# Kernel optimization log

Measured on AMD Instinct MI355X. Metric: run time of the kernel, lower is better.

The kernel has to match this reference:

```python
import jax, jax.numpy as jnp
import numpy as np

NVAR, B, C, H, W = 3, 4, 256, 64, 64
C1 = C // 2          # dat channels (nc)
C2 = C - C1
HEADS = 4
HC = C1 // HEADS     # head channels
STRIDE = 4
KS = 4
HK, WK = H // STRIDE, W // STRIDE
NS = HK * WK         # n_sample
RPE_H, RPE_W = 2 * H - 1, 2 * W - 1
NPAIR = 3


def _grid_sample(img, grid):
    # img [B,C,Hi,Wi]; grid [B,Hg,Wg,2] = (x,y) in [-1,1]; bilinear, align_corners=True, zero-pad
    Bn, Cn, Hi, Wi = img.shape
    x = (grid[..., 0] + 1.0) * 0.5 * (Wi - 1)
    y = (grid[..., 1] + 1.0) * 0.5 * (Hi - 1)
    x0 = jnp.floor(x)
    y0 = jnp.floor(y)
    wx = x - x0
    wy = y - y0
    x0i = x0.astype(jnp.int32)
    y0i = y0.astype(jnp.int32)
    imt = img.transpose(0, 2, 3, 1)  # [B,Hi,Wi,C]
    bidx = jnp.arange(Bn)[:, None, None]

    def corner(yi, xi, wgt):
        ok = ((xi >= 0) & (xi < Wi) & (yi >= 0) & (yi < Hi)).astype(img.dtype)
        val = imt[bidx, jnp.clip(yi, 0, Hi - 1), jnp.clip(xi, 0, Wi - 1)]  # [B,Hg,Wg,C]
        return val * (wgt * ok)[..., None]

    out = (corner(y0i, x0i, (1 - wx) * (1 - wy))
           + corner(y0i, x0i + 1, wx * (1 - wy))
           + corner(y0i + 1, x0i, (1 - wx) * wy)
           + corner(y0i + 1, x0i + 1, wx * wy))
    return out.transpose(0, 3, 1, 2)  # [B,C,Hg,Wg]


def _ref_points(hk, wk):
    # normalized sampling-grid reference points, (y,x) order
    ry = (jnp.linspace(0.5, hk - 0.5, hk) / (hk - 1.0)) * 2.0 - 1.0
    rx = (jnp.linspace(0.5, wk - 0.5, wk) / (wk - 1.0)) * 2.0 - 1.0
    return jnp.stack(jnp.meshgrid(ry, rx, indexing='ij'), axis=-1)  # [hk,wk,2]


def _q_grid(h, w):
    gy = (jnp.arange(h, dtype=jnp.float32) / (h - 1.0)) * 2.0 - 1.0
    gx = (jnp.arange(w, dtype=jnp.float32) / (w - 1.0)) * 2.0 - 1.0
    return jnp.stack(jnp.meshgrid(gy, gx, indexing='ij'), axis=-1).reshape(h * w, 2)


def _conv1x1(x, w, b=None):
    y = jnp.einsum('oc,bchw->bohw', w, x)
    return y if b is None else y + b[None, :, None, None]


def _dat_block(q_in, kv_in, pWq, pbq, pWk, pbk, pWv, pbv, pWo, pbo,
               pdw_w, pdw_b, pln_g, pln_b, ppw_w, prpe):
    Bn = q_in.shape[0]
    q = _conv1x1(q_in, pWq, pbq)  # [B,C1,H,W]
    # offset net: depthwise 4x4 stride-4 conv -> channel LN -> GELU -> 1x1 conv to 2
    off = jax.lax.conv_general_dilated(
        q, pdw_w, (STRIDE, STRIDE), 'VALID',
        dimension_numbers=('NCHW', 'OIHW', 'NCHW'),
        feature_group_count=C1) + pdw_b[None, :, None, None]  # [B,C1,HK,WK]
    mu = off.mean(axis=1, keepdims=True)
    var = ((off - mu) ** 2).mean(axis=1, keepdims=True)
    off = (off - mu) * jax.lax.rsqrt(var + 1e-5) * pln_g[None, :, None, None] + pln_b[None, :, None, None]
    off = jax.nn.gelu(off, approximate=False)
    offset = _conv1x1(off, ppw_w).transpose(0, 2, 3, 1)  # [B,HK,WK,2] (dy,dx)
    # offset_range_factor = -1 -> no tanh scaling, clamp pos into [-1,1]
    pos = jnp.clip(offset + _ref_points(HK, WK)[None], -1.0, 1.0)  # [B,HK,WK,2]
    xs = _grid_sample(kv_in, pos[..., ::-1])  # sample kv at deformed points -> [B,C1,HK,WK]
    k = _conv1x1(xs, pWk, pbk).reshape(Bn, HEADS, HC, NS)
    v = _conv1x1(xs, pWv, pbv).reshape(Bn, HEADS, HC, NS)
    qh = q.reshape(Bn, HEADS, HC, H * W)
    attn = jnp.einsum('bhcm,bhcn->bhmn', qh, k) * (HC ** -0.5)  # [B,h,HW,NS]
    # relative position bias sampled from rpe table
    disp = (_q_grid(H, W)[None, :, None, :] - pos.reshape(Bn, 1, NS, 2)) * 0.5  # [B,HW,NS,2]
    rpe_b = jnp.broadcast_to(prpe[None], (Bn, HEADS, RPE_H, RPE_W))
    bias = _grid_sample(rpe_b, disp[..., ::-1])  # [B,h,HW,NS]
    attn = jax.nn.softmax(attn + bias, axis=-1)
    out = jnp.einsum('bhmn,bhcn->bhcm', attn, v).reshape(Bn, C1, H, W)
    return _conv1x1(out, pWo, pbo)


def _forward(xs, params):
    results = []
    num = 0
    for i in range(NVAR):
        res = xs[i]
        for j in range(i):
            attn_out = _dat_block(xs[i][:, :C1], xs[j][:, :C1],
                                  *(p[num] for p in params))
            # torch: res -= -cat(zeros[:,:C2], attn)  => add attn on channels C2:
            res = res.at[:, C2:].add(attn_out)
            num += 1
        results.append(res)
    return jnp.stack(results)  # [NVAR,B,C,H,W]


def setup_inputs() -> dict:
    key = jax.random.key(0)
    ks = jax.random.split(key, 4)
    d = {}
    for n, k in zip(['x0', 'x1', 'x2'], jax.random.split(ks[0], 3)):
        d[n] = jax.random.normal(k, (B, C, H, W), jnp.float32)

    def w(k, shape, s=0.02):
        return jax.random.normal(k, shape, jnp.float32) * s

    kk = jax.random.split(ks[1], 8)
    d['Wq'] = w(kk[0], (NPAIR, C1, C1))
    d['bq'] = jnp.zeros((NPAIR, C1), jnp.float32)
    d['Wk'] = w(kk[1], (NPAIR, C1, C1))
    d['bk'] = jnp.zeros((NPAIR, C1), jnp.float32)
    d['Wv'] = w(kk[2], (NPAIR, C1, C1))
    d['bv'] = jnp.zeros((NPAIR, C1), jnp.float32)
    d['Wo'] = w(kk[3], (NPAIR, C1, C1))
    d['bo'] = jnp.zeros((NPAIR, C1), jnp.float32)
    d['dw_w'] = w(kk[4], (NPAIR, C1, 1, KS, KS), 0.1)
    d['dw_b'] = jnp.zeros((NPAIR, C1), jnp.float32)
    d['ln_g'] = jnp.ones((NPAIR, C1), jnp.float32)
    d['ln_b'] = jnp.zeros((NPAIR, C1), jnp.float32)
    d['pw_w'] = w(kk[5], (NPAIR, 2, C1), 0.1)
    d['rpe'] = w(kk[6], (NPAIR, HEADS, RPE_H, RPE_W), 0.01)
    return d


def reference(x0, x1, x2, Wq, bq, Wk, bk, Wv, bv, Wo, bo,
              dw_w, dw_b, ln_g, ln_b, pw_w, rpe):
    params = (Wq, bq, Wk, bk, Wv, bv, Wo, bo, dw_w, dw_b, ln_g, ln_b, pw_w, rpe)
    out = _forward([x0, x1, x2], params)
    flow = jnp.zeros((NVAR, x0.shape[0]), out.dtype)
    return out, flow
```

## Files before the change

### kernel.cpp

```cpp
#include <hip/hip_runtime.h>
#include <math.h>

#define NVAR 3
#define BB 4
#define CC 256
#define C1 128
#define HEADS 4
#define HH 64
#define WW 64
#define HW 4096
#define RPE_W 127
#define NP 3
#define SCALE 0.17677669529663687f

typedef short bf16x8 __attribute__((ext_vector_type(8)));
typedef float f32x4 __attribute__((ext_vector_type(4)));
typedef __bf16 bf16x2 __attribute__((ext_vector_type(2)));

__device__ __forceinline__ unsigned short f2bf(float f) {
    unsigned int u = __float_as_uint(f);
    u += 0x7fffu + ((u >> 16) & 1u);
    return (unsigned short)(u >> 16);
}
__device__ __forceinline__ float bflo(unsigned u) { return __uint_as_float(u << 16); }
__device__ __forceinline__ float bfhi(unsigned u) { return __uint_as_float(u & 0xffff0000u); }

__device__ __forceinline__ float dot2bf(unsigned a, unsigned b, float c) {
#if __has_builtin(__builtin_amdgcn_fdot2_f32_bf16)
    return __builtin_amdgcn_fdot2_f32_bf16(__builtin_bit_cast(bf16x2, a),
                                           __builtin_bit_cast(bf16x2, b), c, false);
#else
    return c + bflo(a) * bflo(b) + bfhi(a) * bfhi(b);
#endif
}

__global__ __launch_bounds__(256) void prep_copy(const float* __restrict__ rpe,
                                                 const float* __restrict__ Wq,
                                                 const float* __restrict__ Wo,
                                                 const float* __restrict__ Wk,
                                                 const float* __restrict__ Wv,
                                                 const float* __restrict__ x0,
                                                 unsigned short* __restrict__ tabbf,
                                                 unsigned short* __restrict__ wqh,
                                                 unsigned short* __restrict__ wql,
                                                 unsigned short* __restrict__ woh,
                                                 unsigned short* __restrict__ wkh,
                                                 unsigned short* __restrict__ wvh,
                                                 float* __restrict__ out) {
    int blk = blockIdx.x;
    if (blk >= 24) {
        const long long n4 = (long long)BB * CC * HW / 4;
        long long i = (long long)(blk - 24) * 256 + threadIdx.x;
        const long long stride = 1024LL * 256;
        for (; i < n4 + 12; i += stride) {
            if (i < n4) ((float4*)out)[i] = ((const float4*)x0)[i];
            else out[3LL * BB * CC * HW + (i - n4)] = 0.f;
        }
        return;
    }
    if (blk < 12) {
        const float* src = rpe + (long long)blk * RPE_W * RPE_W;
        unsigned short* dst = tabbf + (long long)blk * 16384;
        for (int idx = threadIdx.x; idx < 16384; idx += 256) {
            int y = idx >> 7, x = idx & 127;
            float v = (y < RPE_W && x < RPE_W) ? src[y * RPE_W + x] : 0.f;
            dst[idx] = f2bf(v);
        }
    } else if (blk < 15) {
        int p = blk - 12;
        for (int i = threadIdx.x; i < 16384; i += 256) {
            float w = Wq[p * 16384 + i];
            unsigned short h = f2bf(w);
            wqh[p * 16384 + i] = h;
            wql[p * 16384 + i] = f2bf(w - bflo((unsigned)h));
        }
    } else if (blk < 18) {
        int p = blk - 15;
        for (int i = threadIdx.x; i < 16384; i += 256)
            woh[p * 16384 + i] = f2bf(Wo[p * 16384 + i]);
    } else if (blk < 21) {
        int p = blk - 18;
        for (int i = threadIdx.x; i < 16384; i += 256)
            wkh[p * 16384 + i] = f2bf(Wk[p * 16384 + i]);
    } else {
        int p = blk - 21;
        for (int i = threadIdx.x; i < 16384; i += 256)
            wvh[p * 16384 + i] = f2bf(Wv[p * 16384 + i]);
    }
}

__global__ __launch_bounds__(256) void conv_q(const float* __restrict__ x1,
                                              const float* __restrict__ x2,
                                              const unsigned short* __restrict__ wqh,
                                              const unsigned short* __restrict__ wql,
                                              const float* __restrict__ bq,
                                              float* __restrict__ qbuf,
                                              unsigned short* __restrict__ qbf,
                                              float* __restrict__ out) {
    __shared__ unsigned short qlds[4][16][136];
    int wid = threadIdx.x >> 6, lane = threadIdx.x & 63;
    int g = lane >> 4, lm = lane & 15;
    int gw = blockIdx.x * 4 + wid;
    int mt = gw & 255;
    int pb = gw >> 8;
    int p = pb >> 2, b = pb & 3;
    const float* X = ((p == 0) ? x1 : x2) + (long long)b * CC * HW;
    int m = mt * 16 + lm;
    float* outc = (p < 2)
        ? out + (((long long)((p + 1) * 4 + b)) * CC) * HW + m
        : nullptr;

    bf16x8 bhi[4], blo[4];
#pragma unroll
    for (int ksl = 0; ksl < 4; ksl++) {
        float v[8];
#pragma unroll
        for (int j = 0; j < 8; j++) {
            int k = ksl * 32 + 8 * g + j;
            v[j] = X[(long long)k * HW + m];
            if (outc) outc[(long long)k * HW] = v[j];
        }
        union { unsigned u[4]; bf16x8 v; } H, L;
#pragma unroll
        for (int t = 0; t < 4; t++) {
            unsigned short h0 = f2bf(v[2 * t]), h1 = f2bf(v[2 * t + 1]);
            unsigned short l0 = f2bf(v[2 * t] - bflo((unsigned)h0));
            unsigned short l1 = f2bf(v[2 * t + 1] - bflo((unsigned)h1));
            H.u[t] = (unsigned)h0 | ((unsigned)h1 << 16);
            L.u[t] = (unsigned)l0 | ((unsigned)l1 << 16);
        }
        bhi[ksl] = H.v;
        blo[ksl] = L.v;
    }

    const unsigned short* WH = wqh + p * 16384;
    const unsigned short* WL = wql + p * 16384;
    unsigned short* ql = &qlds[wid][lm][0];
    f32x4 zero = {0.f, 0.f, 0.f, 0.f};
#pragma unroll
    for (int ct2 = 0; ct2 < 4; ct2++) {
        int ct0 = 2 * ct2, ct1 = ct0 + 1;
        f32x4 a0 = zero, a1 = zero;
#pragma unroll
        for (int ksl = 0; ksl < 4; ksl++) {
            bf16x8 Ah0 = *(const bf16x8*)(WH + (ct0 * 16 + lm) * 128 + ksl * 32 + 8 * g);
            bf16x8 Al0 = *(const bf16x8*)(WL + (ct0 * 16 + lm) * 128 + ksl * 32 + 8 * g);
            bf16x8 Ah1 = *(const bf16x8*)(WH + (ct1 * 16 + lm) * 128 + ksl * 32 + 8 * g);
            bf16x8 Al1 = *(const bf16x8*)(WL + (ct1 * 16 + lm) * 128 + ksl * 32 + 8 * g);
            a0 = __builtin_amdgcn_mfma_f32_16x16x32_bf16(Ah0, bhi[ksl], a0, 0, 0, 0);
            a1 = __builtin_amdgcn_mfma_f32_16x16x32_bf16(Ah1, bhi[ksl], a1, 0, 0, 0);
            a0 = __builtin_amdgcn_mfma_f32_16x16x32_bf16(Ah0, blo[ksl], a0, 0, 0, 0);
            a1 = __builtin_amdgcn_mfma_f32_16x16x32_bf16(Ah1, blo[ksl], a1, 0, 0, 0);
            a0 = __builtin_amdgcn_mfma_f32_16x16x32_bf16(Al0, bhi[ksl], a0, 0, 0, 0);
            a1 = __builtin_amdgcn_mfma_f32_16x16x32_bf16(Al1, bhi[ksl], a1, 0, 0, 0);
        }
        float q0[4], q1[4];
#pragma unroll
        for (int r = 0; r < 4; r++) {
            int c0 = ct0 * 16 + 4 * g + r, c1 = ct1 * 16 + 4 * g + r;
            q0[r] = a0[r] + bq[p * 128 + c0];
            q1[r] = a1[r] + bq[p * 128 + c1];
            qbuf[((long long)pb * 128 + c0) * HW + m] = q0[r];
            qbuf[((long long)pb * 128 + c1) * HW + m] = q1[r];
        }
        *(unsigned*)(ql + ct0 * 16 + 4 * g) =
            (unsigned)f2bf(q0[0] * SCALE) | ((unsigned)f2bf(q0[1] * SCALE) << 16);
        *(unsigned*)(ql + ct0 * 16 + 4 * g + 2) =
            (unsigned)f2bf(q0[2] * SCALE) | ((unsigned)f2bf(q0[3] * SCALE) << 16);
        *(unsigned*)(ql + ct1 * 16 + 4 * g) =
            (unsigned)f2bf(q1[0] * SCALE) | ((unsigned)f2bf(q1[1] * SCALE) << 16);
        *(unsigned*)(ql + ct1 * 16 + 4 * g + 2) =
            (unsigned)f2bf(q1[2] * SCALE) | ((unsigned)f2bf(q1[3] * SCALE) << 16);
    }

    unsigned short* Yb = qbf + ((long long)pb * HW + mt * 16) * 128;
    int q = lane >> 4, cg = lane & 15;
#pragma unroll
    for (int i = 0; i < 4; i++) {
        int row = i * 4 + q;
        uint4 vv = *(const uint4*)&qlds[wid][row][cg * 8];
        *(uint4*)(Yb + row * 128 + cg * 8) = vv;
    }
}

__global__ __launch_bounds__(256) void mid_kernel(const float* __restrict__ qbuf,
                                                  const float* __restrict__ dw_w,
                                                  const float* __restrict__ dw_b,
                                                  const float* __restrict__ ln_g,
                                                  const float* __restrict__ ln_b,
                                                  const float* __restrict__ pw_w,
                                                  const float* __restrict__ x0,
                                                  const float* __restrict__ x1,
                                                  float* __restrict__ posb,
                                                  uint4* __restrict__ prmb,
                                                  unsigned short* __restrict__ xT) {
    __shared__ float sm[32 * 4 * 65 + 16 * 128];
    int blk = blockIdx.x;
    int tid = threadIdx.x;
    if (blk < 192) {
        float (*ld)[4][65] = (float(*)[4][65])sm;
        float (*dwout)[128] = (float(*)[128])(sm + 32 * 4 * 65);
        int pb = blk >> 4, hk = blk & 15;
        int p = pb >> 2;
        for (int cq = 0; cq < 4; cq++) {
            int c32 = cq * 32;
            __syncthreads();
#pragma unroll
            for (int it = 0; it < 8; it++) {
                int i2 = tid + it * 256;
                int c = i2 >> 6, rem = i2 & 63;
                int y = rem >> 4, xq = rem & 15;
                float4 v = *(const float4*)(qbuf + ((long long)pb * 128 + c32 + c) * HW
                                            + (4 * hk + y) * 64 + xq * 4);
                ld[c][y][xq * 4 + 0] = v.x;
                ld[c][y][xq * 4 + 1] = v.y;
                ld[c][y][xq * 4 + 2] = v.z;
                ld[c][y][xq * 4 + 3] = v.w;
            }
            __syncthreads();
            int wk = tid >> 4;
#pragma unroll
            for (int oi = 0; oi < 2; oi++) {
                int c = (tid & 15) + oi * 16;
                const float* dwp = dw_w + (p * 128 + c32 + c) * 16;
                float acc = dw_b[p * 128 + c32 + c];
#pragma unroll
                for (int ky = 0; ky < 4; ky++)
#pragma unroll
                    for (int kx = 0; kx < 4; kx++)
                        acc += ld[c][ky][wk * 4 + kx] * dwp[ky * 4 + kx];
                dwout[wk][c32 + c] = acc;
            }
        }
        __syncthreads();
        int wid = tid >> 6, lane = tid & 63;
        for (int i = 0; i < 4; i++) {
            int wk = wid * 4 + i;
            int s = hk * 16 + wk;
            float a0 = dwout[wk][lane], a1 = dwout[wk][lane + 64];
            float s1 = a0 + a1;
#pragma unroll
            for (int o = 1; o < 64; o <<= 1) s1 += __shfl_xor(s1, o);
            float mu = s1 * (1.f / 128.f);
            float d0 = a0 - mu, d1 = a1 - mu;
            float v2 = d0 * d0 + d1 * d1;
#pragma unroll
            for (int o = 1; o < 64; o <<= 1) v2 += __shfl_xor(v2, o);
            float rs = rsqrtf(v2 * (1.f / 128.f) + 1e-5f);
            int c0 = lane, c1 = lane + 64;
            float y0 = d0 * rs * ln_g[p * 128 + c0] + ln_b[p * 128 + c0];
            float y1 = d1 * rs * ln_g[p * 128 + c1] + ln_b[p * 128 + c1];
            float g0 = 0.5f * y0 * (1.f + erff(y0 * 0.70710678118654752f));
            float g1 = 0.5f * y1 * (1.f + erff(y1 * 0.70710678118654752f));
            float o0 = pw_w[(p * 2 + 0) * 128 + c0] * g0
                     + pw_w[(p * 2 + 0) * 128 + c1] * g1;
            float o1 = pw_w[(p * 2 + 1) * 128 + c0] * g0
                     + pw_w[(p * 2 + 1) * 128 + c1] * g1;
#pragma unroll
            for (int o = 1; o < 64; o <<= 1) o0 += __shfl_xor(o0, o);
#pragma unroll
            for (int o = 1; o < 64; o <<= 1) o1 += __shfl_xor(o1, o);
            if (lane == 0) {
                int wk2 = s & 15;
                float refy = (hk + 0.5f) * (2.f / 15.f) - 1.f;
                float refx = (wk2 + 0.5f) * (2.f / 15.f) - 1.f;
                float py = fminf(fmaxf(o0 + refy, -1.f), 1.f);
                float px = fminf(fmaxf(o1 + refx, -1.f), 1.f);
                int pbn = pb * 256 + s;
                posb[pbn * 2 + 0] = py;
                posb[pbn * 2 + 1] = px;
                float cy = 31.5f * (1.f - py), cx = 31.5f * (1.f - px);
                float yf = floorf(cy), xf = floorf(cx);
                float wy = cy - yf, wx = cx - xf;
                int Y0 = (int)yf, X0 = (int)xf;
                uint4 v;
                v.x = (unsigned)f2bf((1.f - wy) * (1.f - wx))
                    | ((unsigned)f2bf((1.f - wy) * wx) << 16);
                v.y = (unsigned)f2bf(wy * (1.f - wx))
                    | ((unsigned)f2bf(wy * wx) << 16);
                v.z = (unsigned)((Y0 * 128 + X0) * 2);
                v.w = 0;
                prmb[pbn] = v;
            }
        }
    } else {
        float (*ld2)[65] = (float(*)[65])sm;
        int rem = blk - 192;
        int v = rem >> 10;
        int rem1 = rem & 1023;
        int b = rem1 >> 8;
        int rem2 = rem1 & 255;
        int ct = rem2 >> 6;
        int mt = rem2 & 63;
        const float* src = ((v == 0) ? x0 : x1) + (long long)b * CC * HW
                           + (long long)(ct * 32) * HW + mt * 64;
#pragma unroll
        for (int it = 0; it < 2; it++) {
            int c = tid >> 3, x4 = (tid & 7) + it * 8;
            float4 w = *(const float4*)(src + (long long)c * HW + x4 * 4);
            ld2[c][x4 * 4 + 0] = w.x;
            ld2[c][x4 * 4 + 1] = w.y;
            ld2[c][x4 * 4 + 2] = w.z;
            ld2[c][x4 * 4 + 3] = w.w;
        }
        __syncthreads();
        int m = tid >> 2, cg = tid & 3;
        union { unsigned u[4]; } pk;
#pragma unroll
        for (int t = 0; t < 4; t++) {
            unsigned short h0 = f2bf(ld2[cg * 8 + 2 * t][m]);
            unsigned short h1 = f2bf(ld2[cg * 8 + 2 * t + 1][m]);
            pk.u[t] = (unsigned)h0 | ((unsigned)h1 << 16);
        }
        *(uint4*)(xT + (((long long)(v * 4 + b)) * HW + mt * 64 + m) * 128
                  + ct * 32 + cg * 8) = *(uint4*)pk.u;
    }
}

__global__ __launch_bounds__(256) void sample_kv(const unsigned short* __restrict__ xT,
                                                 const float* __restrict__ posb,
                                                 const unsigned short* __restrict__ wkh,
                                                 const unsigned short* __restrict__ wvh,
                                                 const float* __restrict__ bk,
                                                 const float* __restrict__ bv,
                                                 unsigned short* __restrict__ kbf,
                                                 unsigned short* __restrict__ vbf) {
    __shared__ unsigned short xls[32 * 128];
    int blk = blockIdx.x;
    int pb = blk >> 3;
    int nt = blk & 7;
    int p = pb >> 2, b = pb & 3;
    int n0 = nt * 32;
    int tid = threadIdx.x;

    {
        int nl = tid >> 3, co = tid & 7;
        int n = n0 + nl;
        float py = posb[(pb * 256 + n) * 2 + 0];
        float px = posb[(pb * 256 + n) * 2 + 1];
        float yi = (py + 1.f) * 31.5f, xi = (px + 1.f) * 31.5f;
        yi = fminf(fmaxf(yi, 0.f), 63.f);
        xi = fminf(fmaxf(xi, 0.f), 63.f);
        int y0 = min((int)yi, 62);
        int x0i = min((int)xi, 62);
        float wy = yi - (float)y0, wx = xi - (float)x0i;
        float w00 = (1.f - wy) * (1.f - wx), w01 = (1.f - wy) * wx;
        float w10 = wy * (1.f - wx), w11 = wy * wx;
        int vsel = (p == 2) ? 1 : 0;
        const unsigned short* base = xT + ((long long)(vsel * 4 + b)) * HW * 128;
        int m00 = y0 * 64 + x0i;
        char* dst = (char*)xls;
#pragma unroll
        for (int cb = 0; cb < 2; cb++) {
            int c0 = co * 16 + cb * 8;
            bf16x8 a = *(const bf16x8*)(base + (long long)m00 * 128 + c0);
            bf16x8 bb = *(const bf16x8*)(base + (long long)(m00 + 1) * 128 + c0);
            bf16x8 cc = *(const bf16x8*)(base + (long long)(m00 + 64) * 128 + c0);
            bf16x8 dd = *(const bf16x8*)(base + (long long)(m00 + 65) * 128 + c0);
            union { unsigned u[4]; bf16x8 v; } R;
#pragma unroll
            for (int t = 0; t < 4; t++) {
                float r0 = w00 * bflo((unsigned)(unsigned short)a[2 * t])
                         + w01 * bflo((unsigned)(unsigned short)bb[2 * t])
                         + w10 * bflo((unsigned)(unsigned short)cc[2 * t])
                         + w11 * bflo((unsigned)(unsigned short)dd[2 * t]);
                float r1 = w00 * bflo((unsigned)(unsigned short)a[2 * t + 1])
                         + w01 * bflo((unsigned)(unsigned short)bb[2 * t + 1])
                         + w10 * bflo((unsigned)(unsigned short)cc[2 * t + 1])
                         + w11 * bflo((unsigned)(unsigned short)dd[2 * t + 1]);
                R.u[t] = (unsigned)f2bf(r0) | ((unsigned)f2bf(r1) << 16);
            }
            *(bf16x8*)(dst + ((nl * 256 + c0 * 2) ^ ((nl & 7) << 4))) = R.v;
        }
    }
    __syncthreads();

    int wid = tid >> 6, lane = tid & 63;
    int g = lane >> 4, lm = lane & 15;
    int ntile = wid & 1, isv = wid >> 1;
    int nl = ntile * 16 + lm;
    const char* srcl = (const char*)xls;
    bf16x8 xf[4];
#pragma unroll
    for (int ks = 0; ks < 4; ks++)
        xf[ks] = *(const bf16x8*)(srcl + ((nl * 256 + (ks * 32 + 8 * g) * 2)
                                          ^ ((nl & 7) << 4)));
    f32x4 zero = {0.f, 0.f, 0.f, 0.f};
    if (!isv) {
        const unsigned short* WK = wkh + p * 16384;
#pragma unroll
        for (int ct = 0; ct < 8; ct++) {
            f32x4 acc = zero;
#pragma unroll
            for (int ks = 0; ks < 4; ks++) {
                bf16x8 wf = *(const bf16x8*)(WK + (ct * 16 + lm) * 128 + ks * 32 + 8 * g);
                acc = __builtin_amdgcn_mfma_f32_16x16x32_bf16(xf[ks], wf, acc, 0, 0, 0);
            }
            float bias = bk[p * 128 + ct * 16 + lm];
#pragma unroll
            for (int r = 0; r < 4; r++) {
                int n = n0 + ntile * 16 + 4 * g + r;
                kbf[((long long)pb * 256 + n) * 128 + ct * 16 + lm] = f2bf(acc[r] + bias);
            }
        }
    } else {
        const unsigned short* WV = wvh + p * 16384;
#pragma unroll
        for (int ct = 0; ct < 8; ct++) {
            f32x4 acc = zero;
#pragma unroll
            for (int ks = 0; ks < 4; ks++) {
                bf16x8 wf = *(const bf16x8*)(WV + (ct * 16 + lm) * 128 + ks * 32 + 8 * g);
                acc = __builtin_amdgcn_mfma_f32_16x16x32_bf16(wf, xf[ks], acc, 0, 0, 0);
            }
#pragma unroll
            for (int r = 0; r < 4; r++) {
                int c = ct * 16 + 4 * g + r;
                vbf[((long long)pb * 128 + c) * 256 + n0 + ntile * 16 + lm]
                    = f2bf(acc[r] + bv[p * 128 + c]);
            }
        }
    }
}

__global__ __launch_bounds__(256, 4) void attn_mfma(
        const unsigned short* __restrict__ qbf,
        const unsigned short* __restrict__ kbf,
        const unsigned short* __restrict__ vbf,
        const unsigned short* __restrict__ tabbf,
        const uint4* __restrict__ prmb,
        unsigned short* __restrict__ obf) {
    __shared__ unsigned short tab[16384 + 8];
    __shared__ uint4 prm[256];
    int tid = threadIdx.x;
    int wid = tid >> 6, lane = tid & 63;
    int g = lane >> 4, lm = lane & 15;
    int bid = blockIdx.x;
    int my = bid & 63;
    int h = (bid >> 6) & 3;
    int b = (bid >> 8) & 3;
    int p = bid >> 10;
    int pb = p * 4 + b;

    {
        const uint4* ts = (const uint4*)(tabbf + (long long)(p * 4 + h) * 16384);
        uint4* td = (uint4*)tab;
#pragma unroll
        for (int i = 0; i < 8; i++) td[tid + i * 256] = ts[tid + i * 256];
        prm[tid] = prmb[pb * 256 + tid];
    }
    __syncthreads();

    int mx = (wid << 4) + lm;

    bf16x8 qf = *(const bf16x8*)(qbf + ((long long)pb * HW + my * 64 + mx) * 128
                                 + h * 32 + 8 * g);
    const unsigned short* kbase = kbf + ((long long)pb * 256 + lm) * 128
                                  + h * 32 + 8 * g;
    f32x4 zero = {0.f, 0.f, 0.f, 0.f};
    f32x4 acc[16];
    __builtin_amdgcn_s_setprio(1);
#pragma unroll
    for (int ni = 0; ni < 16; ni++) {
        bf16x8 kf = *(const bf16x8*)(kbase + ni * 16 * 128);
        acc[ni] = __builtin_amdgcn_mfma_f32_16x16x32_bf16(kf, qf, zero, 0, 0, 0);
    }
    __builtin_amdgcn_s_setprio(0);

    int laneoff = (my * 128 + mx) * 2;
    const char* tb = (const char*)tab;
#pragma unroll
    for (int ni = 0; ni < 16; ni++) {
#pragma unroll
        for (int r = 0; r < 4; r++) {
            int n = ni * 16 + 4 * g + r;
            uint4 pw = prm[n];
            int va = (int)pw.z + laneoff;
            int va4 = va & ~3;
            int sh = va & 3;
            unsigned r0 = *(const unsigned*)(tb + va4);
            unsigned r1 = *(const unsigned*)(tb + va4 + 4);
            unsigned r2 = *(const unsigned*)(tb + va4 + 256);
            unsigned r3 = *(const unsigned*)(tb + va4 + 260);
            unsigned p0 = __builtin_amdgcn_alignbyte(r1, r0, sh);
            unsigned p1 = __builtin_amdgcn_alignbyte(r3, r2, sh);
            float t = acc[ni][r];
            t = dot2bf(p0, pw.x, t);
            t = dot2bf(p1, pw.y, t);
            acc[ni][r] = t;
        }
    }

    float mxv = -1e30f;
#pragma unroll
    for (int ni = 0; ni < 16; ni++)
        mxv = fmaxf(mxv, fmaxf(fmaxf(acc[ni][0], acc[ni][1]),
                               fmaxf(acc[ni][2], acc[ni][3])));
    mxv = fmaxf(mxv, __shfl_xor(mxv, 16));
    mxv = fmaxf(mxv, __shfl_xor(mxv, 32));
    float sum = 0.f;
    unsigned dwA[16], dwB[16];
#pragma unroll
    for (int ni = 0; ni < 16; ni++) {
        float e0 = __expf(acc[ni][0] - mxv);
        float e1 = __expf(acc[ni][1] - mxv);
        float e2 = __expf(acc[ni][2] - mxv);
        float e3 = __expf(acc[ni][3] - mxv);
        sum += (e0 + e1) + (e2 + e3);
        asm("v_cvt_pk_bf16_f32 %0, %1, %2" : "=v"(dwA[ni]) : "v"(e0), "v"(e1));
        asm("v_cvt_pk_bf16_f32 %0, %1, %2" : "=v"(dwB[ni]) : "v"(e2), "v"(e3));
    }
    sum += __shfl_xor(sum, 16);
    sum += __shfl_xor(sum, 32);

    int src0 = ((g & 1) << 5) + lm;
    int src1 = src0 + 16;
    bool sel = (g >> 1) != 0;
    const unsigned short* vb0 = vbf + ((long long)pb * 128 + h * 32 + lm) * 256
                                + 8 * g;
    f32x4 o0 = zero, o1 = zero;
#pragma unroll
    for (int st = 0; st < 8; st++) {
        unsigned d0a = __shfl(dwA[2 * st], src0), d0b = __shfl(dwA[2 * st + 1], src0);
        unsigned d1a = __shfl(dwB[2 * st], src0), d1b = __shfl(dwB[2 * st + 1], src0);
        unsigned d2a = __shfl(dwA[2 * st], src1), d2b = __shfl(dwA[2 * st + 1], src1);
        unsigned d3a = __shfl(dwB[2 * st], src1), d3b = __shfl(dwB[2 * st + 1], src1);
        union { unsigned u[4]; bf16x8 v; } pf;
        pf.u[0] = sel ? d0b : d0a;
        pf.u[1] = sel ? d1b : d1a;
        pf.u[2] = sel ? d2b : d2a;
        pf.u[3] = sel ? d3b : d3a;
        bf16x8 v0 = *(const bf16x8*)(vb0 + st * 32);
        bf16x8 v1 = *(const bf16x8*)(vb0 + 4096 + st * 32);
        __builtin_amdgcn_s_setprio(1);
        o0 = __builtin_amdgcn_mfma_f32_16x16x32_bf16(v0, pf.v, o0, 0, 0, 0);
        o1 = __builtin_amdgcn_mfma_f32_16x16x32_bf16(v1, pf.v, o1, 0, 0, 0);
        __builtin_amdgcn_s_setprio(0);
    }

    float inv = 1.f / sum;
    __syncthreads();
    {
        unsigned short* rw = tab + wid * 640 + lm * 40;
        *(unsigned*)(rw + g * 4) =
            (unsigned)f2bf(o0[0] * inv) | ((unsigned)f2bf(o0[1] * inv) << 16);
        *(unsigned*)(rw + g * 4 + 2) =
            (unsigned)f2bf(o0[2] * inv) | ((unsigned)f2bf(o0[3] * inv) << 16);
        *(unsigned*)(rw + 16 + g * 4) =
            (unsigned)f2bf(o1[0] * inv) | ((unsigned)f2bf(o1[1] * inv) << 16);
        *(unsigned*)(rw + 16 + g * 4 + 2) =
            (unsigned)f2bf(o1[2] * inv) | ((unsigned)f2bf(o1[3] * inv) << 16);
    }
    int row = lane >> 2, cb = lane & 3;
    uint4 vv = *(const uint4*)(tab + wid * 640 + row * 40 + cb * 8);
    *(uint4*)(obf + ((long long)pb * HW + my * 64 + wid * 16 + row) * 128
              + h * 32 + cb * 8) = vv;
}

__global__ __launch_bounds__(256) void conv_wo(const float* __restrict__ x1,
                                               const float* __restrict__ x2,
                                               const unsigned short* __restrict__ obf,
                                               const unsigned short* __restrict__ woh,
                                               const float* __restrict__ bo,
                                               float* __restrict__ out) {
    int wid = threadIdx.x >> 6, lane = threadIdx.x & 63;
    int g = lane >> 4, lm = lane & 15;
    int gw = blockIdx.x * 4 + wid;
    int mt = gw & 255;
    int b = (gw >> 8) & 3;
    int vs = gw >> 10;
    int m = mt * 16 + lm;
    int np = vs + 1;

    f32x4 acc[8];
#pragma unroll
    for (int ct = 0; ct < 8; ct++) acc[ct] = (f32x4){0.f, 0.f, 0.f, 0.f};

    for (int pi = 0; pi < np; pi++) {
        int p = vs ? (1 + pi) : 0;
        const unsigned short* Om = obf + ((long long)(p * 4 + b) * HW + m) * 128;
        const unsigned short* WH = woh + p * 16384;
#pragma unroll
        for (int ksl = 0; ksl < 4; ksl++) {
            bf16x8 bh = *(const bf16x8*)(Om + ksl * 32 + 8 * g);
#pragma unroll
            for (int ct = 0; ct < 8; ct++) {
                bf16x8 A = *(const bf16x8*)(WH + (ct * 16 + lm) * 128 + ksl * 32 + 8 * g);
                acc[ct] = __builtin_amdgcn_mfma_f32_16x16x32_bf16(A, bh, acc[ct], 0, 0, 0);
            }
        }
    }

    int qi = vs + 1;
    const float* xq = (vs ? x2 : x1) + (long long)b * CC * HW;
#pragma unroll
    for (int ct = 0; ct < 8; ct++)
#pragma unroll
        for (int r = 0; r < 4; r++) {
            int c = ct * 16 + 4 * g + r;
            float bias = vs ? (bo[128 + c] + bo[256 + c]) : bo[c];
            float base = xq[(long long)(128 + c) * HW + m];
            out[(((long long)(qi * 4 + b)) * CC + 128 + c) * HW + m]
                = base + acc[ct][r] + bias;
        }
}

extern "C" void kernel_launch(void* const* d_in, const int* in_sizes, int n_in,
                              void* d_out, int out_size, void* d_ws, size_t ws_size,
                              hipStream_t stream) {
    const float* x0 = (const float*)d_in[0];
    const float* x1 = (const float*)d_in[1];
    const float* x2 = (const float*)d_in[2];
    const float* Wq = (const float*)d_in[3];
    const float* bq = (const float*)d_in[4];
    const float* Wk = (const float*)d_in[5];
    const float* bk = (const float*)d_in[6];
    const float* Wv = (const float*)d_in[7];
    const float* bv = (const float*)d_in[8];
    const float* Wo = (const float*)d_in[9];
    const float* bo = (const float*)d_in[10];
    const float* dw_w = (const float*)d_in[11];
    const float* dw_b = (const float*)d_in[12];
    const float* ln_g = (const float*)d_in[13];
    const float* ln_b = (const float*)d_in[14];
    const float* pw_w = (const float*)d_in[15];
    const float* rpe = (const float*)d_in[16];
    float* out = (float*)d_out;

    float* ws = (float*)d_ws;
    float* qbuf = ws;
    unsigned short* obf = (unsigned short*)ws;
    float* posb = ws + 6291456;
    unsigned short* xT = (unsigned short*)(posb + 6144);
    unsigned short* qbf = xT + 4194304;
    unsigned short* kbf = qbf + 12582912;
    unsigned short* vbf = kbf + 393216;
    unsigned short* tabbf = vbf + 393216;
    uint4* prmb = (uint4*)(tabbf + 196608);
    unsigned short* wqh = (unsigned short*)(prmb + 3072);
    unsigned short* wql = wqh + 49152;
    unsigned short* woh = wql + 49152;
    unsigned short* wkh = woh + 49152;
    unsigned short* wvh = wkh + 49152;

    prep_copy<<<1048, 256, 0, stream>>>(rpe, Wq, Wo, Wk, Wv, x0, tabbf,
                                        wqh, wql, woh, wkh, wvh, out);
    conv_q<<<768, 256, 0, stream>>>(x1, x2, wqh, wql, bq, qbuf, qbf, out);
    mid_kernel<<<2240, 256, 0, stream>>>(qbuf, dw_w, dw_b, ln_g, ln_b, pw_w,
                                         x0, x1, posb, prmb, xT);
    sample_kv<<<96, 256, 0, stream>>>(xT, posb, wkh, wvh, bk, bv, kbf, vbf);
    attn_mfma<<<3072, 256, 0, stream>>>(qbf, kbf, vbf, tabbf, prmb, obf);
    conv_wo<<<512, 256, 0, stream>>>(x1, x2, obf, woh, bo, out);
}
```

Measured before the change: 178.9 us.

## Drop split-bf16 Q projection, share x2 loads across pairs, feed offset conv from bf16 q

The Q 1x1 conv now uses a single bf16 MFMA pass instead of the hi/lo three-pass split. Pairs 1 and 2, which both read x2, are merged into one wave so the input is loaded and converted once, cutting the grid from 768 to 512 blocks. The fp32 qbuf intermediate is removed. The offset-net depthwise conv in mid_kernel now reads the scaled bf16 q buffer and undoes the scale on the weights. This lowers MFMA work and memory traffic, but the offsets are now computed at lower precision, which can shift the sampling positions.

```diff
diff --git a/kernel.cpp b/kernel.cpp
--- a/kernel.cpp
+++ b/kernel.cpp
@@ -42,7 +42,6 @@
                                                  const float* __restrict__ x0,
                                                  unsigned short* __restrict__ tabbf,
                                                  unsigned short* __restrict__ wqh,
-                                                 unsigned short* __restrict__ wql,
                                                  unsigned short* __restrict__ woh,
                                                  unsigned short* __restrict__ wkh,
                                                  unsigned short* __restrict__ wvh,
@@ -68,12 +67,8 @@
         }
     } else if (blk < 15) {
         int p = blk - 12;
-        for (int i = threadIdx.x; i < 16384; i += 256) {
-            float w = Wq[p * 16384 + i];
-            unsigned short h = f2bf(w);
-            wqh[p * 16384 + i] = h;
-            wql[p * 16384 + i] = f2bf(w - bflo((unsigned)h));
-        }
+        for (int i = threadIdx.x; i < 16384; i += 256)
+            wqh[p * 16384 + i] = f2bf(Wq[p * 16384 + i]);
     } else if (blk < 18) {
         int p = blk - 15;
         for (int i = threadIdx.x; i < 16384; i += 256)
@@ -92,9 +87,7 @@
 __global__ __launch_bounds__(256) void conv_q(const float* __restrict__ x1,
                                               const float* __restrict__ x2,
                                               const unsigned short* __restrict__ wqh,
-                                              const unsigned short* __restrict__ wql,
                                               const float* __restrict__ bq,
-                                              float* __restrict__ qbuf,
                                               unsigned short* __restrict__ qbf,
                                               float* __restrict__ out) {
     __shared__ unsigned short qlds[4][16][136];
@@ -102,15 +95,15 @@
     int g = lane >> 4, lm = lane & 15;
     int gw = blockIdx.x * 4 + wid;
     int mt = gw & 255;
-    int pb = gw >> 8;
-    int p = pb >> 2, b = pb & 3;
-    const float* X = ((p == 0) ? x1 : x2) + (long long)b * CC * HW;
+    int pbi = gw >> 8;
+    int merged = pbi >> 2;
+    int b = pbi & 3;
+    const float* X = (merged ? x2 : x1) + (long long)b * CC * HW;
     int m = mt * 16 + lm;
-    float* outc = (p < 2)
-        ? out + (((long long)((p + 1) * 4 + b)) * CC) * HW + m
-        : nullptr;
-
-    bf16x8 bhi[4], blo[4];
+    int qi = merged + 1;
+    float* outc = out + (((long long)(qi * 4 + b)) * CC) * HW + m;
+
+    bf16x8 bh[4];
 #pragma unroll
     for (int ksl = 0; ksl < 4; ksl++) {
         float v[8];
@@ -118,72 +111,60 @@
         for (int j = 0; j < 8; j++) {
             int k = ksl * 32 + 8 * g + j;
             v[j] = X[(long long)k * HW + m];
-            if (outc) outc[(long long)k * HW] = v[j];
-        }
-        union { unsigned u[4]; bf16x8 v; } H, L;
-#pragma unroll
-        for (int t = 0; t < 4; t++) {
-            unsigned short h0 = f2bf(v[2 * t]), h1 = f2bf(v[2 * t + 1]);
-            unsigned short l0 = f2bf(v[2 * t] - bflo((unsigned)h0));
-            unsigned short l1 = f2bf(v[2 * t + 1] - bflo((unsigned)h1));
-            H.u[t] = (unsigned)h0 | ((unsigned)h1 << 16);
-            L.u[t] = (unsigned)l0 | ((unsigned)l1 << 16);
-        }
-        bhi[ksl] = H.v;
-        blo[ksl] = L.v;
-    }
-
-    const unsigned short* WH = wqh + p * 16384;
-    const unsigned short* WL = wql + p * 16384;
+            outc[(long long)k * HW] = v[j];
+        }
+        union { unsigned u[4]; bf16x8 v; } H;
+#pragma unroll
+        for (int t = 0; t < 4; t++)
+            H.u[t] = (unsigned)f2bf(v[2 * t]) | ((unsigned)f2bf(v[2 * t + 1]) << 16);
+        bh[ksl] = H.v;
+    }
+
+    f32x4 zero = {0.f, 0.f, 0.f, 0.f};
     unsigned short* ql = &qlds[wid][lm][0];
-    f32x4 zero = {0.f, 0.f, 0.f, 0.f};
-#pragma unroll
-    for (int ct2 = 0; ct2 < 4; ct2++) {
-        int ct0 = 2 * ct2, ct1 = ct0 + 1;
-        f32x4 a0 = zero, a1 = zero;
-#pragma unroll
-        for (int ksl = 0; ksl < 4; ksl++) {
-            bf16x8 Ah0 = *(const bf16x8*)(WH + (ct0 * 16 + lm) * 128 + ksl * 32 + 8 * g);
-            bf16x8 Al0 = *(const bf16x8*)(WL + (ct0 * 16 + lm) * 128 + ksl * 32 + 8 * g);
-            bf16x8 Ah1 = *(const bf16x8*)(WH + (ct1 * 16 + lm) * 128 + ksl * 32 + 8 * g);
-            bf16x8 Al1 = *(const bf16x8*)(WL + (ct1 * 16 + lm) * 128 + ksl * 32 + 8 * g);
-            a0 = __builtin_amdgcn_mfma_f32_16x16x32_bf16(Ah0, bhi[ksl], a0, 0, 0, 0);
-            a1 = __builtin_amdgcn_mfma_f32_16x16x32_bf16(Ah1, bhi[ksl], a1, 0, 0, 0);
-            a0 = __builtin_amdgcn_mfma_f32_16x16x32_bf16(Ah0, blo[ksl], a0, 0, 0, 0);
-            a1 = __builtin_amdgcn_mfma_f32_16x16x32_bf16(Ah1, blo[ksl], a1, 0, 0, 0);
-            a0 = __builtin_amdgcn_mfma_f32_16x16x32_bf16(Al0, bhi[ksl], a0, 0, 0, 0);
-            a1 = __builtin_amdgcn_mfma_f32_16x16x32_bf16(Al1, bhi[ksl], a1, 0, 0, 0);
-        }
-        float q0[4], q1[4];
-#pragma unroll
-        for (int r = 0; r < 4; r++) {
-            int c0 = ct0 * 16 + 4 * g + r, c1 = ct1 * 16 + 4 * g + r;
-            q0[r] = a0[r] + bq[p * 128 + c0];
-            q1[r] = a1[r] + bq[p * 128 + c1];
-            qbuf[((long long)pb * 128 + c0) * HW + m] = q0[r];
-            qbuf[((long long)pb * 128 + c1) * HW + m] = q1[r];
-        }
-        *(unsigned*)(ql + ct0 * 16 + 4 * g) =
-            (unsigned)f2bf(q0[0] * SCALE) | ((unsigned)f2bf(q0[1] * SCALE) << 16);
-        *(unsigned*)(ql + ct0 * 16 + 4 * g + 2) =
-            (unsigned)f2bf(q0[2] * SCALE) | ((unsigned)f2bf(q0[3] * SCALE) << 16);
-        *(unsigned*)(ql + ct1 * 16 + 4 * g) =
-            (unsigned)f2bf(q1[0] * SCALE) | ((unsigned)f2bf(q1[1] * SCALE) << 16);
-        *(unsigned*)(ql + ct1 * 16 + 4 * g + 2) =
-            (unsigned)f2bf(q1[2] * SCALE) | ((unsigned)f2bf(q1[3] * SCALE) << 16);
-    }
-
-    unsigned short* Yb = qbf + ((long long)pb * HW + mt * 16) * 128;
-    int q = lane >> 4, cg = lane & 15;
-#pragma unroll
-    for (int i = 0; i < 4; i++) {
-        int row = i * 4 + q;
-        uint4 vv = *(const uint4*)&qlds[wid][row][cg * 8];
-        *(uint4*)(Yb + row * 128 + cg * 8) = vv;
-    }
-}
-
-__global__ __launch_bounds__(256) void mid_kernel(const float* __restrict__ qbuf,
+    int qq = lane >> 4, cg = lane & 15;
+
+    for (int rep = 0; rep <= merged; rep++) {
+        int p = merged ? (1 + rep) : 0;
+        int pb = p * 4 + b;
+        const unsigned short* WH = wqh + p * 16384;
+#pragma unroll
+        for (int ct2 = 0; ct2 < 4; ct2++) {
+            int ct0 = 2 * ct2, ct1 = ct0 + 1;
+            f32x4 a0 = zero, a1 = zero;
+#pragma unroll
+            for (int ksl = 0; ksl < 4; ksl++) {
+                bf16x8 Ah0 = *(const bf16x8*)(WH + (ct0 * 16 + lm) * 128 + ksl * 32 + 8 * g);
+                bf16x8 Ah1 = *(const bf16x8*)(WH + (ct1 * 16 + lm) * 128 + ksl * 32 + 8 * g);
+                a0 = __builtin_amdgcn_mfma_f32_16x16x32_bf16(Ah0, bh[ksl], a0, 0, 0, 0);
+                a1 = __builtin_amdgcn_mfma_f32_16x16x32_bf16(Ah1, bh[ksl], a1, 0, 0, 0);
+            }
+            float q0[4], q1[4];
+#pragma unroll
+            for (int r = 0; r < 4; r++) {
+                q0[r] = a0[r] + bq[p * 128 + ct0 * 16 + 4 * g + r];
+                q1[r] = a1[r] + bq[p * 128 + ct1 * 16 + 4 * g + r];
+            }
+            *(unsigned*)(ql + ct0 * 16 + 4 * g) =
+                (unsigned)f2bf(q0[0] * SCALE) | ((unsigned)f2bf(q0[1] * SCALE) << 16);
+            *(unsigned*)(ql + ct0 * 16 + 4 * g + 2) =
+                (unsigned)f2bf(q0[2] * SCALE) | ((unsigned)f2bf(q0[3] * SCALE) << 16);
+            *(unsigned*)(ql + ct1 * 16 + 4 * g) =
+                (unsigned)f2bf(q1[0] * SCALE) | ((unsigned)f2bf(q1[1] * SCALE) << 16);
+            *(unsigned*)(ql + ct1 * 16 + 4 * g + 2) =
+                (unsigned)f2bf(q1[2] * SCALE) | ((unsigned)f2bf(q1[3] * SCALE) << 16);
+        }
+        unsigned short* Yb = qbf + ((long long)pb * HW + mt * 16) * 128;
+#pragma unroll
+        for (int i = 0; i < 4; i++) {
+            int row = i * 4 + qq;
+            uint4 vv = *(const uint4*)&qlds[wid][row][cg * 8];
+            *(uint4*)(Yb + row * 128 + cg * 8) = vv;
+        }
+    }
+}
+
+__global__ __launch_bounds__(256) void mid_kernel(const unsigned short* __restrict__ qbf,
                                                   const float* __restrict__ dw_w,
                                                   const float* __restrict__ dw_b,
                                                   const float* __restrict__ ln_g,
@@ -194,44 +175,50 @@
                                                   float* __restrict__ posb,
                                                   uint4* __restrict__ prmb,
                                                   unsigned short* __restrict__ xT) {
-    __shared__ float sm[32 * 4 * 65 + 16 * 128];
+    __shared__ char sm[40960];
     int blk = blockIdx.x;
     int tid = threadIdx.x;
     if (blk < 192) {
-        float (*ld)[4][65] = (float(*)[4][65])sm;
-        float (*dwout)[128] = (float(*)[128])(sm + 32 * 4 * 65);
+        unsigned short* qs = (unsigned short*)sm;
+        float (*dwout)[128] = (float(*)[128])(sm + 32768);
         int pb = blk >> 4, hk = blk & 15;
         int p = pb >> 2;
-        for (int cq = 0; cq < 4; cq++) {
-            int c32 = cq * 32;
+        int c = tid & 127;
+        int wk0 = tid >> 7;
+        const float* dwp_g = dw_w + (p * 128 + c) * 16;
+        float dwp[16];
+#pragma unroll
+        for (int j = 0; j < 16; j++) dwp[j] = dwp_g[j] * (1.f / SCALE);
+        float acc[8];
+#pragma unroll
+        for (int o = 0; o < 8; o++) acc[o] = dw_b[p * 128 + c];
+        const unsigned short* Q = qbf + ((long long)pb * HW + hk * 256) * 128;
+        for (int pass = 0; pass < 2; pass++) {
             __syncthreads();
 #pragma unroll
             for (int it = 0; it < 8; it++) {
-                int i2 = tid + it * 256;
-                int c = i2 >> 6, rem = i2 & 63;
-                int y = rem >> 4, xq = rem & 15;
-                float4 v = *(const float4*)(qbuf + ((long long)pb * 128 + c32 + c) * HW
-                                            + (4 * hk + y) * 64 + xq * 4);
-                ld[c][y][xq * 4 + 0] = v.x;
-                ld[c][y][xq * 4 + 1] = v.y;
-                ld[c][y][xq * 4 + 2] = v.z;
-                ld[c][y][xq * 4 + 3] = v.w;
+                int idx = tid + it * 256;
+                int mloc = idx >> 4, cg = idx & 15;
+                *(uint4*)(qs + mloc * 128 + cg * 8) =
+                    *(const uint4*)(Q + (long long)(pass * 128 + mloc) * 128 + cg * 8);
             }
             __syncthreads();
-            int wk = tid >> 4;
-#pragma unroll
-            for (int oi = 0; oi < 2; oi++) {
-                int c = (tid & 15) + oi * 16;
-                const float* dwp = dw_w + (p * 128 + c32 + c) * 16;
-                float acc = dw_b[p * 128 + c32 + c];
-#pragma unroll
-                for (int ky = 0; ky < 4; ky++)
+#pragma unroll
+            for (int o = 0; o < 8; o++) {
+                int wk = wk0 + o * 2;
+                float a = acc[o];
+#pragma unroll
+                for (int kyl = 0; kyl < 2; kyl++)
 #pragma unroll
                     for (int kx = 0; kx < 4; kx++)
-                        acc += ld[c][ky][wk * 4 + kx] * dwp[ky * 4 + kx];
-                dwout[wk][c32 + c] = acc;
-            }
-        }
+                        a += bflo((unsigned)qs[(kyl * 64 + wk * 4 + kx) * 128 + c])
+                             * dwp[(pass * 2 + kyl) * 4 + kx];
+                acc[o] = a;
+            }
+        }
+        __syncthreads();
+#pragma unroll
+        for (int o = 0; o < 8; o++) dwout[wk0 + o * 2][c] = acc[o];
         __syncthreads();
         int wid = tid >> 6, lane = tid & 63;
         for (int i = 0; i < 4; i++) {
@@ -628,7 +615,6 @@
     float* out = (float*)d_out;
 
     float* ws = (float*)d_ws;
-    float* qbuf = ws;
     unsigned short* obf = (unsigned short*)ws;
     float* posb = ws + 6291456;
     unsigned short* xT = (unsigned short*)(posb + 6144);
@@ -638,15 +624,14 @@
     unsigned short* tabbf = vbf + 393216;
     uint4* prmb = (uint4*)(tabbf + 196608);
     unsigned short* wqh = (unsigned short*)(prmb + 3072);
-    unsigned short* wql = wqh + 49152;
-    unsigned short* woh = wql + 49152;
+    unsigned short* woh = wqh + 49152;
     unsigned short* wkh = woh + 49152;
     unsigned short* wvh = wkh + 49152;
 
     prep_copy<<<1048, 256, 0, stream>>>(rpe, Wq, Wo, Wk, Wv, x0, tabbf,
-                                        wqh, wql, woh, wkh, wvh, out);
-    conv_q<<<768, 256, 0, stream>>>(x1, x2, wqh, wql, bq, qbuf, qbf, out);
-    mid_kernel<<<2240, 256, 0, stream>>>(qbuf, dw_w, dw_b, ln_g, ln_b, pw_w,
+                                        wqh, woh, wkh, wvh, out);
+    conv_q<<<512, 256, 0, stream>>>(x1, x2, wqh, bq, qbf, out);
+    mid_kernel<<<2240, 256, 0, stream>>>(qbf, dw_w, dw_b, ln_g, ln_b, pw_w,
                                          x0, x1, posb, prmb, xT);
     sample_kv<<<96, 256, 0, stream>>>(xT, posb, wkh, wvh, bk, bv, kbf, vbf);
     attn_mfma<<<3072, 256, 0, stream>>>(qbf, kbf, vbf, tabbf, prmb, obf);
```

New measurement: 163.1 us. 8.8% less time.
